# Kernel tuning notes

Measured on AMD Instinct MI355X. Metric: run time of the kernel, lower is better.

## Reference

```python
import jax, jax.numpy as jnp
import numpy as np

B, T, S, F, D, M = 8, 8192, 8192, 64, 64, 128
EPS = 1e-9


def _draw_omega(n_omega, d_feature, rng):
    # Stacked orthogonal blocks scaled by sqrt(d_feature), as in the TF module.
    n_blocks = (n_omega + d_feature - 1) // d_feature + 1
    blocks = []
    for _ in range(n_blocks):
        g = rng.standard_normal((d_feature, d_feature)).astype(np.float32)
        q, _ = np.linalg.qr(g)
        blocks.append(q * np.sqrt(float(d_feature)))
    return jnp.asarray(np.concatenate(blocks, axis=0)[:n_omega])


def setup_inputs() -> dict:
    k0 = jax.random.key(0)
    kq, kv, kk = jax.random.split(k0, 3)
    query = jax.random.normal(kq, (B, T, F), dtype=jnp.float32)
    value = jax.random.normal(kv, (B, S, D), dtype=jnp.float32)
    key = jax.random.normal(kk, (B, S, F), dtype=jnp.float32)
    omega = _draw_omega(M, F, np.random.default_rng(0))  # (M, F)
    return {"query": query, "value": value, "key": key, "omega": omega}


def _phi(x, omega):
    # x: (B, L, F) -> (B, L, 2M) positive random features
    m = omega.shape[0]
    square_sum = jnp.sum(x * x, axis=-1, keepdims=True) / 2.0  # (B, L, 1)
    xw = jnp.einsum('blf,mf->blm', x, omega)                   # (B, L, M)
    unnorm = jnp.exp(jnp.concatenate([xw, -xw], axis=-1) - square_sum) + EPS
    return unnorm / jnp.sqrt(2.0 * m)


def reference(query, value, key, omega):
    q = _phi(query, omega)  # (B, T, 2M)
    k = _phi(key, omega)    # (B, S, 2M)
    ones = jnp.ones(value.shape[:-1] + (1,), dtype=value.dtype)
    v1 = jnp.concatenate([value, ones], axis=-1)               # (B, S, D+1)
    kv = jnp.einsum('bsm,bsd->bmd', k, v1)                     # (B, 2M, D+1)
    qkv = jnp.einsum('btm,bmd->btd', q, kv)                    # (B, T, D+1)
    normalizer = qkv[:, :, -1:]
    return qkv[:, :, :-1] / normalizer
```

## Files before the change

### kernel.cpp

```cpp
#include <hip/hip_runtime.h>


constexpr int NB = 8;
constexpr int NT = 8192;
constexpr float EPSF = 1e-9f;
constexpr float SCALE = 0.0625f;

typedef short s8v __attribute__((ext_vector_type(8)));
typedef short s4v __attribute__((ext_vector_type(4)));
typedef float f4v __attribute__((ext_vector_type(4)));

__device__ inline f4v mfma16(s8v a, s8v b, f4v c) {
  return __builtin_amdgcn_mfma_f32_16x16x32_bf16(a, b, c, 0, 0, 0);
}

__device__ inline short bf16_rne(float f) {
  unsigned u = __builtin_bit_cast(unsigned, f);
  u += 0x7fffu + ((u >> 16) & 1u);
  return (short)(u >> 16);
}
__device__ inline float bf16_to_f(short h) {
  unsigned u = ((unsigned)(unsigned short)h) << 16;
  return __builtin_bit_cast(float, u);
}

__global__ void setup_omega(const float* __restrict__ omega,
                            short* __restrict__ oh, short* __restrict__ ol) {
  int i = blockIdx.x * 256 + threadIdx.x;
  if (i >= 128 * 64) return;
  float w = omega[i];
  short h = bf16_rne(w);
  oh[i] = h;
  ol[i] = bf16_rne(w - bf16_to_f(h));
}

struct PhiRows {
  s8v ah0, al0, ah1, al1;
  float ssr[4];
  float ss;
};

__device__ inline void split8(f4v a, f4v b, s8v& h, s8v& l) {
  float v[8] = {a.x, a.y, a.z, a.w, b.x, b.y, b.z, b.w};
#pragma unroll
  for (int j = 0; j < 8; ++j) {
    short hh = bf16_rne(v[j]);
    h[j] = hh;
    l[j] = bf16_rne(v[j] - bf16_to_f(hh));
  }
}

__device__ inline void load_phi_rows(const float* __restrict__ xrow_base, int lane, PhiRows& P) {
  const int r = lane & 15, q = lane >> 4;
  const float* p = xrow_base + r * 64 + q * 8;
  f4v u0 = *(const f4v*)(p);
  f4v u1 = *(const f4v*)(p + 4);
  f4v u2 = *(const f4v*)(p + 32);
  f4v u3 = *(const f4v*)(p + 36);
  float ss = u0.x * u0.x + u0.y * u0.y + u0.z * u0.z + u0.w * u0.w
           + u1.x * u1.x + u1.y * u1.y + u1.z * u1.z + u1.w * u1.w
           + u2.x * u2.x + u2.y * u2.y + u2.z * u2.z + u2.w * u2.w
           + u3.x * u3.x + u3.y * u3.y + u3.z * u3.z + u3.w * u3.w;
  ss += __shfl_xor(ss, 16, 64);
  ss += __shfl_xor(ss, 32, 64);
  ss *= 0.5f;
  P.ss = ss;
#pragma unroll
  for (int reg = 0; reg < 4; ++reg) P.ssr[reg] = __shfl(ss, q * 4 + reg, 64);
  split8(u0, u1, P.ah0, P.al0);
  split8(u2, u3, P.ah1, P.al1);
}

__device__ inline f4v phi_xw_tile(const PhiRows& P, const short* __restrict__ oh,
                                  const short* __restrict__ ol, int f0, int lane) {
  const int fr = f0 + (lane & 15);
  const int q = lane >> 4;
  s8v bh0 = *(const s8v*)(oh + fr * 64 + q * 8);
  s8v bh1 = *(const s8v*)(oh + fr * 64 + 32 + q * 8);
  s8v bl0 = *(const s8v*)(ol + fr * 64 + q * 8);
  s8v bl1 = *(const s8v*)(ol + fr * 64 + 32 + q * 8);
  f4v c = {0.f, 0.f, 0.f, 0.f};
  c = mfma16(P.ah0, bh0, c);
  c = mfma16(P.ah1, bh1, c);
  c = mfma16(P.al0, bh0, c);
  c = mfma16(P.al1, bh1, c);
  c = mfma16(P.ah0, bl0, c);
  c = mfma16(P.ah1, bl1, c);
  return c;
}

__device__ inline f4v phi_xw_tile_T(const PhiRows& P, const short* __restrict__ oh,
                                    const short* __restrict__ ol, int f0, int lane) {
  const int fr = f0 + (lane & 15);
  const int q = lane >> 4;
  s8v ah0 = *(const s8v*)(oh + fr * 64 + q * 8);
  s8v ah1 = *(const s8v*)(oh + fr * 64 + 32 + q * 8);
  s8v al0 = *(const s8v*)(ol + fr * 64 + q * 8);
  s8v al1 = *(const s8v*)(ol + fr * 64 + 32 + q * 8);
  f4v c = {0.f, 0.f, 0.f, 0.f};
  c = mfma16(ah0, P.ah0, c);
  c = mfma16(ah1, P.ah1, c);
  c = mfma16(al0, P.ah0, c);
  c = mfma16(al1, P.ah1, c);
  c = mfma16(ah0, P.al0, c);
  c = mfma16(ah1, P.al1, c);
  return c;
}

constexpr int KF_P = 72;
constexpr int QF_P = 264;
constexpr int PART_SZ = 65 * 256;

__global__ __launch_bounds__(256, 2) void kv_fused(
    const float* __restrict__ key, const float* __restrict__ value,
    const short* __restrict__ oh, const short* __restrict__ ol,
    short* __restrict__ partial, float* __restrict__ kvacc, int use_partial) {
  __shared__ short kft[256 * KF_P];
  __shared__ short v1t[80 * KF_P];
  const int tid = threadIdx.x, lane = tid & 63, w = tid >> 6;
  const int b = blockIdx.x >> 6;
  const int s0 = (blockIdx.x & 63) * 128;
  const int q = lane >> 4, r15 = lane & 15;

  for (int i = tid; i < 15 * KF_P; i += 256) v1t[65 * KF_P + i] = 0;

  f4v acc[4][5];
#pragma unroll
  for (int j = 0; j < 4; ++j)
#pragma unroll
    for (int n = 0; n < 5; ++n) acc[j][n] = f4v{0.f, 0.f, 0.f, 0.f};

  for (int sc = 0; sc < 2; ++sc) {
    const int sbase = s0 + sc * 64;
    __syncthreads();
    {
      const float* vb = value + ((size_t)b * NT + sbase) * 64;
#pragma unroll
      for (int i = 0; i < 4; ++i) {
        int e4 = tid + i * 256;
        f4v v4 = ((const f4v*)vb)[e4];
        int s = e4 >> 4, d0 = (e4 & 15) * 4;
        v1t[(d0 + 0) * KF_P + s] = bf16_rne(v4.x);
        v1t[(d0 + 1) * KF_P + s] = bf16_rne(v4.y);
        v1t[(d0 + 2) * KF_P + s] = bf16_rne(v4.z);
        v1t[(d0 + 3) * KF_P + s] = bf16_rne(v4.w);
      }
      if (tid < 64) v1t[64 * KF_P + tid] = (short)0x3F80;
    }
    {
      PhiRows P;
      load_phi_rows(key + ((size_t)b * NT + sbase + w * 16) * 64, lane, P);
#pragma unroll
      for (int ft = 0; ft < 8; ++ft) {
        f4v c = phi_xw_tile(P, oh, ol, ft * 16, lane);
        s4v pk, nk;
#pragma unroll
        for (int reg = 0; reg < 4; ++reg) {
          float xw = c[reg];
          pk[reg] = bf16_rne((__expf(xw - P.ssr[reg]) + EPSF) * SCALE);
          nk[reg] = bf16_rne((__expf(-xw - P.ssr[reg]) + EPSF) * SCALE);
        }
        const int scol = w * 16 + q * 4;
        *(s4v*)(kft + (ft * 16 + r15) * KF_P + scol) = pk;
        *(s4v*)(kft + (128 + ft * 16 + r15) * KF_P + scol) = nk;
      }
    }
    __syncthreads();
#pragma unroll
    for (int ks = 0; ks < 2; ++ks) {
      s8v bf[5];
#pragma unroll
      for (int n = 0; n < 5; ++n)
        bf[n] = *(const s8v*)(v1t + (n * 16 + r15) * KF_P + ks * 32 + q * 8);
#pragma unroll
      for (int j = 0; j < 4; ++j) {
        s8v a = *(const s8v*)(kft + (w * 64 + j * 16 + r15) * KF_P + ks * 32 + q * 8);
#pragma unroll
        for (int n = 0; n < 5; ++n) acc[j][n] = mfma16(a, bf[n], acc[j][n]);
      }
    }
  }
  if (use_partial) {
    short* pb = partial + (size_t)blockIdx.x * PART_SZ;
#pragma unroll
    for (int j = 0; j < 4; ++j) {
      int m = w * 64 + j * 16 + q * 4;
#pragma unroll
      for (int n = 0; n < 4; ++n) {
        int d = n * 16 + r15;
        s4v pk;
#pragma unroll
        for (int reg = 0; reg < 4; ++reg) pk[reg] = bf16_rne(acc[j][n][reg]);
        *(s4v*)(pb + d * 256 + m) = pk;
      }
      if (r15 == 0) {
        s4v pk;
#pragma unroll
        for (int reg = 0; reg < 4; ++reg) pk[reg] = bf16_rne(acc[j][4][reg]);
        *(s4v*)(pb + 64 * 256 + m) = pk;
      }
    }
  } else {
    float* pb = kvacc + (size_t)b * PART_SZ;
#pragma unroll
    for (int j = 0; j < 4; ++j) {
      int m = w * 64 + j * 16 + q * 4;
#pragma unroll
      for (int n = 0; n < 4; ++n) {
        int d = n * 16 + r15;
#pragma unroll
        for (int reg = 0; reg < 4; ++reg) atomicAdd(pb + d * 256 + m + reg, acc[j][n][reg]);
      }
      if (r15 == 0)
#pragma unroll
        for (int reg = 0; reg < 4; ++reg) atomicAdd(pb + 64 * 256 + m + reg, acc[j][4][reg]);
    }
  }
}

__global__ __launch_bounds__(256) void kv_finalize(
    const short* __restrict__ partial, const float* __restrict__ kvacc,
    short* __restrict__ kvfrag, int use_partial) {
  int i = blockIdx.x * 256 + threadIdx.x;
  int b = i / 20480;
  int rem = i - b * 20480;
  int d = rem >> 8;
  int m = rem & 255;
  float s = 0.f;
  if (d < 65) {
    if (use_partial) {
      const short* p = partial + (size_t)(b * 64) * PART_SZ + d * 256 + m;
#pragma unroll 8
      for (int c = 0; c < 64; ++c) s += bf16_to_f(p[(size_t)c * PART_SZ]);
    } else {
      s = kvacc[(size_t)b * PART_SZ + d * 256 + m];
    }
  }
  int ks = m >> 5, qq = (m >> 3) & 3, j = m & 7;
  int n = d >> 4, r = d & 15;
  int lane = qq * 16 + r;
  kvfrag[(((size_t)b * 40 + ks * 5 + n) * 64 + lane) * 8 + j] = bf16_rne(s);
}

__global__ __launch_bounds__(256, 4) void qkv_fused(
    const float* __restrict__ query, const short* __restrict__ oh,
    const short* __restrict__ ol, const short* __restrict__ kvfrag,
    float* __restrict__ out) {
  __shared__ __align__(16) short qf[64 * QF_P];
  const int tid = threadIdx.x, lane = tid & 63, w = tid >> 6;
  const int b = blockIdx.x >> 7;
  const int t0 = (blockIdx.x & 127) * 64;
  const int q = lane >> 4, r15 = lane & 15;

  {
    PhiRows P;
    load_phi_rows(query + ((size_t)b * NT + t0 + w * 16) * 64, lane, P);
    const int t_loc = w * 16 + r15;
#pragma unroll
    for (int ft = 0; ft < 8; ++ft) {
      f4v c = phi_xw_tile_T(P, oh, ol, ft * 16, lane);
      s4v pk, nk;
#pragma unroll
      for (int reg = 0; reg < 4; ++reg) {
        float xw = c[reg];
        pk[reg] = bf16_rne((__expf(xw - P.ss) + EPSF) * SCALE);
        nk[reg] = bf16_rne((__expf(-xw - P.ss) + EPSF) * SCALE);
      }
      *(s4v*)(qf + t_loc * QF_P + ft * 16 + q * 4) = pk;
      *(s4v*)(qf + t_loc * QF_P + 128 + ft * 16 + q * 4) = nk;
    }
  }
  f4v acc[5];
#pragma unroll
  for (int n = 0; n < 5; ++n) acc[n] = f4v{0.f, 0.f, 0.f, 0.f};
  const short* kvb = kvfrag + (size_t)b * 40 * 512;
#pragma unroll
  for (int ks = 0; ks < 8; ++ks) {
    s8v a = *(const s8v*)(qf + (w * 16 + r15) * QF_P + ks * 32 + q * 8);
#pragma unroll
    for (int n = 0; n < 5; ++n) {
      s8v bf = *(const s8v*)(kvb + ((size_t)(ks * 5 + n)) * 512 + lane * 8);
      acc[n] = mfma16(a, bf, acc[n]);
    }
  }
  float den_r[4];
#pragma unroll
  for (int reg = 0; reg < 4; ++reg) den_r[reg] = __shfl(acc[4][reg], lane & 48, 64);
  float* stg = (float*)(qf + w * 16 * QF_P);
#pragma unroll
  for (int n = 0; n < 4; ++n)
#pragma unroll
    for (int reg = 0; reg < 4; ++reg) {
      int row = q * 4 + reg;
      int col = n * 16 + r15;
      stg[row * 68 + col] = acc[n][reg] / den_r[reg];
    }
  float* ob = out + ((size_t)b * NT + t0 + w * 16) * 64;
#pragma unroll
  for (int rr = 0; rr < 4; ++rr) {
    int row = rr * 4 + q;
    int c4 = r15 * 4;
    *(f4v*)(ob + row * 64 + c4) = *(const f4v*)(stg + row * 68 + c4);
  }
}

extern "C" void kernel_launch(void* const* d_in, const int* in_sizes, int n_in,
                              void* d_out, int out_size, void* d_ws, size_t ws_size,
                              hipStream_t stream) {
  const float* query = (const float*)d_in[0];
  const float* value = (const float*)d_in[1];
  const float* key   = (const float*)d_in[2];
  const float* omega = (const float*)d_in[3];
  float* out = (float*)d_out;

  char* ws = (char*)d_ws;
  short* oh = (short*)ws;
  short* ol = (short*)(ws + 16384);
  short* kvfrag = (short*)(ws + 32768);
  short* partial = (short*)(ws + 360448);
  float* kvacc = (float*)(ws + 360448);
  const size_t need_full = 360448 + (size_t)512 * PART_SZ * 2;
  const int use_partial = (ws_size >= need_full) ? 1 : 0;

  setup_omega<<<32, 256, 0, stream>>>(omega, oh, ol);
  if (!use_partial) {
    hipMemsetAsync(kvacc, 0, (size_t)8 * PART_SZ * 4, stream);
  }
  kv_fused<<<512, 256, 0, stream>>>(key, value, oh, ol, partial, kvacc, use_partial);
  kv_finalize<<<640, 256, 0, stream>>>(partial, kvacc, kvfrag, use_partial);
  qkv_fused<<<1024, 256, 0, stream>>>(query, oh, ol, kvfrag, out);
}
```

Before: 143.1 us.

## Replace LDS-staged kv kernel with per-wave register shuffles for MFMA fragments

The block-level kv_fused kernel is replaced by kv_wave. Each wave owns a 128-row chunk and a 32-feature group and builds MFMA B fragments from phi(key) with cross-lane shuffles, while the value A fragments are read straight from global memory into registers. This removes shared memory staging and the __syncthreads barriers, and moves work to smaller 128-thread blocks. In exchange, phi is recomputed per feature group, value is reloaded by four waves each, value reads are strided scalar loads, and partial results are written as scalar stores instead of vector stores.

```diff
diff --git a/kernel.cpp b/kernel.cpp
--- a/kernel.cpp
+++ b/kernel.cpp
@@ -22,6 +22,9 @@
 __device__ inline float bf16_to_f(short h) {
   unsigned u = ((unsigned)(unsigned short)h) << 16;
   return __builtin_bit_cast(float, u);
+}
+__device__ inline unsigned pack2(short lo, short hi) {
+  return (unsigned)(unsigned short)lo | ((unsigned)(unsigned short)hi << 16);
 }
 
 __global__ void setup_omega(const float* __restrict__ omega,
@@ -107,113 +110,119 @@
   return c;
 }
 
-constexpr int KF_P = 72;
-constexpr int QF_P = 264;
-constexpr int PART_SZ = 65 * 256;
-
-__global__ __launch_bounds__(256, 2) void kv_fused(
+__device__ inline s8v bfrag_shuffle(unsigned g0d0, unsigned g0d1,
+                                    unsigned g1d0, unsigned g1d1, int lane) {
+  const int sb = ((lane & 16) ? 32 : 0) | (lane & 15);
+  int a0 = __shfl((int)g0d0, sb, 64);
+  int a1 = __shfl((int)g0d1, sb, 64);
+  int a2 = __shfl((int)g0d0, sb + 16, 64);
+  int a3 = __shfl((int)g0d1, sb + 16, 64);
+  int b0 = __shfl((int)g1d0, sb, 64);
+  int b1 = __shfl((int)g1d1, sb, 64);
+  int b2 = __shfl((int)g1d0, sb + 16, 64);
+  int b3 = __shfl((int)g1d1, sb + 16, 64);
+  const bool hi = lane >= 32;
+  int4 r;
+  r.x = hi ? b0 : a0;
+  r.y = hi ? b1 : a1;
+  r.z = hi ? b2 : a2;
+  r.w = hi ? b3 : a3;
+  return __builtin_bit_cast(s8v, r);
+}
+
+__global__ __launch_bounds__(128, 2) void kv_wave(
     const float* __restrict__ key, const float* __restrict__ value,
     const short* __restrict__ oh, const short* __restrict__ ol,
     short* __restrict__ partial, float* __restrict__ kvacc, int use_partial) {
-  __shared__ short kft[256 * KF_P];
-  __shared__ short v1t[80 * KF_P];
-  const int tid = threadIdx.x, lane = tid & 63, w = tid >> 6;
-  const int b = blockIdx.x >> 6;
-  const int s0 = (blockIdx.x & 63) * 128;
+  const int lane = threadIdx.x & 63;
+  const int wid = blockIdx.x * 2 + (threadIdx.x >> 6);
+  const int b = wid >> 8;
+  const int rem = wid & 255;
+  const int chunk = rem >> 2, fg = rem & 3;
   const int q = lane >> 4, r15 = lane & 15;
 
-  for (int i = tid; i < 15 * KF_P; i += 256) v1t[65 * KF_P + i] = 0;
-
-  f4v acc[4][5];
-#pragma unroll
-  for (int j = 0; j < 4; ++j)
-#pragma unroll
-    for (int n = 0; n < 5; ++n) acc[j][n] = f4v{0.f, 0.f, 0.f, 0.f};
-
-  for (int sc = 0; sc < 2; ++sc) {
-    const int sbase = s0 + sc * 64;
-    __syncthreads();
-    {
-      const float* vb = value + ((size_t)b * NT + sbase) * 64;
-#pragma unroll
-      for (int i = 0; i < 4; ++i) {
-        int e4 = tid + i * 256;
-        f4v v4 = ((const f4v*)vb)[e4];
-        int s = e4 >> 4, d0 = (e4 & 15) * 4;
-        v1t[(d0 + 0) * KF_P + s] = bf16_rne(v4.x);
-        v1t[(d0 + 1) * KF_P + s] = bf16_rne(v4.y);
-        v1t[(d0 + 2) * KF_P + s] = bf16_rne(v4.z);
-        v1t[(d0 + 3) * KF_P + s] = bf16_rne(v4.w);
+  f4v acc[5][4];
+#pragma unroll
+  for (int mt = 0; mt < 5; ++mt)
+#pragma unroll
+    for (int n = 0; n < 4; ++n) acc[mt][n] = f4v{0.f, 0.f, 0.f, 0.f};
+
+  s8v a4;
+  {
+    short v = (r15 == 0) ? (short)0x3F80 : (short)0;
+#pragma unroll
+    for (int j = 0; j < 8; ++j) a4[j] = v;
+  }
+
+  for (int sub = 0; sub < 4; ++sub) {
+    const int sB = chunk * 128 + sub * 32;
+    PhiRows P0, P1;
+    load_phi_rows(key + ((size_t)b * NT + sB) * 64, lane, P0);
+    load_phi_rows(key + ((size_t)b * NT + sB + 16) * 64, lane, P1);
+    s8v aF[4];
+#pragma unroll
+    for (int mt = 0; mt < 4; ++mt) {
+      const float* vp = value + ((size_t)b * NT + sB + q * 8) * 64 + mt * 16 + r15;
+#pragma unroll
+      for (int j = 0; j < 8; ++j) aF[mt][j] = bf16_rne(vp[j * 64]);
+    }
+#pragma unroll
+    for (int ot = 0; ot < 2; ++ot) {
+      const int f0 = fg * 32 + ot * 16;
+      f4v c0 = phi_xw_tile(P0, oh, ol, f0, lane);
+      f4v c1 = phi_xw_tile(P1, oh, ol, f0, lane);
+      short p0s[4], n0s[4], p1s[4], n1s[4];
+#pragma unroll
+      for (int reg = 0; reg < 4; ++reg) {
+        float x0 = c0[reg], x1 = c1[reg];
+        p0s[reg] = bf16_rne((__expf(x0 - P0.ssr[reg]) + EPSF) * SCALE);
+        n0s[reg] = bf16_rne((__expf(-x0 - P0.ssr[reg]) + EPSF) * SCALE);
+        p1s[reg] = bf16_rne((__expf(x1 - P1.ssr[reg]) + EPSF) * SCALE);
+        n1s[reg] = bf16_rne((__expf(-x1 - P1.ssr[reg]) + EPSF) * SCALE);
       }
-      if (tid < 64) v1t[64 * KF_P + tid] = (short)0x3F80;
-    }
-    {
-      PhiRows P;
-      load_phi_rows(key + ((size_t)b * NT + sbase + w * 16) * 64, lane, P);
-#pragma unroll
-      for (int ft = 0; ft < 8; ++ft) {
-        f4v c = phi_xw_tile(P, oh, ol, ft * 16, lane);
-        s4v pk, nk;
+      {
+        s8v bF = bfrag_shuffle(pack2(p0s[0], p0s[1]), pack2(p0s[2], p0s[3]),
+                               pack2(p1s[0], p1s[1]), pack2(p1s[2], p1s[3]), lane);
+#pragma unroll
+        for (int mt = 0; mt < 4; ++mt) acc[mt][ot] = mfma16(aF[mt], bF, acc[mt][ot]);
+        acc[4][ot] = mfma16(a4, bF, acc[4][ot]);
+      }
+      {
+        s8v bF = bfrag_shuffle(pack2(n0s[0], n0s[1]), pack2(n0s[2], n0s[3]),
+                               pack2(n1s[0], n1s[1]), pack2(n1s[2], n1s[3]), lane);
+#pragma unroll
+        for (int mt = 0; mt < 4; ++mt) acc[mt][2 + ot] = mfma16(aF[mt], bF, acc[mt][2 + ot]);
+        acc[4][2 + ot] = mfma16(a4, bF, acc[4][2 + ot]);
+      }
+    }
+  }
+  if (use_partial) {
+    short* pb = partial + ((size_t)(b * 64 + chunk) * 65) * 256;
+#pragma unroll
+    for (int n = 0; n < 4; ++n) {
+      const int m = ((n & 2) ? 128 : 0) + fg * 32 + (n & 1) * 16 + r15;
+#pragma unroll
+      for (int mt = 0; mt < 4; ++mt)
 #pragma unroll
         for (int reg = 0; reg < 4; ++reg) {
-          float xw = c[reg];
-          pk[reg] = bf16_rne((__expf(xw - P.ssr[reg]) + EPSF) * SCALE);
-          nk[reg] = bf16_rne((__expf(-xw - P.ssr[reg]) + EPSF) * SCALE);
+          int d = mt * 16 + q * 4 + reg;
+          pb[d * 256 + m] = bf16_rne(acc[mt][n][reg]);
         }
-        const int scol = w * 16 + q * 4;
-        *(s4v*)(kft + (ft * 16 + r15) * KF_P + scol) = pk;
-        *(s4v*)(kft + (128 + ft * 16 + r15) * KF_P + scol) = nk;
-      }
-    }
-    __syncthreads();
-#pragma unroll
-    for (int ks = 0; ks < 2; ++ks) {
-      s8v bf[5];
-#pragma unroll
-      for (int n = 0; n < 5; ++n)
-        bf[n] = *(const s8v*)(v1t + (n * 16 + r15) * KF_P + ks * 32 + q * 8);
-#pragma unroll
-      for (int j = 0; j < 4; ++j) {
-        s8v a = *(const s8v*)(kft + (w * 64 + j * 16 + r15) * KF_P + ks * 32 + q * 8);
-#pragma unroll
-        for (int n = 0; n < 5; ++n) acc[j][n] = mfma16(a, bf[n], acc[j][n]);
-      }
-    }
-  }
-  if (use_partial) {
-    short* pb = partial + (size_t)blockIdx.x * PART_SZ;
-#pragma unroll
-    for (int j = 0; j < 4; ++j) {
-      int m = w * 64 + j * 16 + q * 4;
-#pragma unroll
-      for (int n = 0; n < 4; ++n) {
-        int d = n * 16 + r15;
-        s4v pk;
-#pragma unroll
-        for (int reg = 0; reg < 4; ++reg) pk[reg] = bf16_rne(acc[j][n][reg]);
-        *(s4v*)(pb + d * 256 + m) = pk;
-      }
-      if (r15 == 0) {
-        s4v pk;
-#pragma unroll
-        for (int reg = 0; reg < 4; ++reg) pk[reg] = bf16_rne(acc[j][4][reg]);
-        *(s4v*)(pb + 64 * 256 + m) = pk;
-      }
+      if (q == 0) pb[64 * 256 + m] = bf16_rne(acc[4][n][0]);
     }
   } else {
-    float* pb = kvacc + (size_t)b * PART_SZ;
-#pragma unroll
-    for (int j = 0; j < 4; ++j) {
-      int m = w * 64 + j * 16 + q * 4;
-#pragma unroll
-      for (int n = 0; n < 4; ++n) {
-        int d = n * 16 + r15;
-#pragma unroll
-        for (int reg = 0; reg < 4; ++reg) atomicAdd(pb + d * 256 + m + reg, acc[j][n][reg]);
-      }
-      if (r15 == 0)
-#pragma unroll
-        for (int reg = 0; reg < 4; ++reg) atomicAdd(pb + 64 * 256 + m + reg, acc[j][4][reg]);
+    float* pb = kvacc + (size_t)b * (65 * 256);
+#pragma unroll
+    for (int n = 0; n < 4; ++n) {
+      const int m = ((n & 2) ? 128 : 0) + fg * 32 + (n & 1) * 16 + r15;
+#pragma unroll
+      for (int mt = 0; mt < 4; ++mt)
+#pragma unroll
+        for (int reg = 0; reg < 4; ++reg) {
+          int d = mt * 16 + q * 4 + reg;
+          atomicAdd(pb + d * 256 + m, acc[mt][n][reg]);
+        }
+      if (q == 0) atomicAdd(pb + 64 * 256 + m, acc[4][n][0]);
     }
   }
 }
@@ -229,11 +238,11 @@
   float s = 0.f;
   if (d < 65) {
     if (use_partial) {
-      const short* p = partial + (size_t)(b * 64) * PART_SZ + d * 256 + m;
+      const short* p = partial + ((size_t)(b * 64) * 65 + d) * 256 + m;
 #pragma unroll 8
-      for (int c = 0; c < 64; ++c) s += bf16_to_f(p[(size_t)c * PART_SZ]);
+      for (int c = 0; c < 64; ++c) s += bf16_to_f(p[(size_t)c * (65 * 256)]);
     } else {
-      s = kvacc[(size_t)b * PART_SZ + d * 256 + m];
+      s = kvacc[((size_t)b * 65 + d) * 256 + m];
     }
   }
   int ks = m >> 5, qq = (m >> 3) & 3, j = m & 7;
@@ -242,6 +251,7 @@
   kvfrag[(((size_t)b * 40 + ks * 5 + n) * 64 + lane) * 8 + j] = bf16_rne(s);
 }
 
+constexpr int QF_P = 264;
 __global__ __launch_bounds__(256, 4) void qkv_fused(
     const float* __restrict__ query, const short* __restrict__ oh,
     const short* __restrict__ ol, const short* __restrict__ kvfrag,
@@ -319,14 +329,14 @@
   short* kvfrag = (short*)(ws + 32768);
   short* partial = (short*)(ws + 360448);
   float* kvacc = (float*)(ws + 360448);
-  const size_t need_full = 360448 + (size_t)512 * PART_SZ * 2;
+  const size_t need_full = 360448 + (size_t)NB * 64 * 65 * 256 * 2;
   const int use_partial = (ws_size >= need_full) ? 1 : 0;
 
   setup_omega<<<32, 256, 0, stream>>>(omega, oh, ol);
   if (!use_partial) {
-    hipMemsetAsync(kvacc, 0, (size_t)8 * PART_SZ * 4, stream);
-  }
-  kv_fused<<<512, 256, 0, stream>>>(key, value, oh, ol, partial, kvacc, use_partial);
+    hipMemsetAsync(kvacc, 0, (size_t)NB * 65 * 256 * 4, stream);
+  }
+  kv_wave<<<1024, 128, 0, stream>>>(key, value, oh, ol, partial, kvacc, use_partial);
   kv_finalize<<<640, 256, 0, stream>>>(partial, kvacc, kvfrag, use_partial);
   qkv_fused<<<1024, 256, 0, stream>>>(query, oh, ol, kvfrag, out);
 }
```

Result: no change. 144.4 us (+0.9%).
